# Kernel optimization log

Measured on AMD Instinct MI355X. Metric: run time of the kernel, lower is better.

Reference implementation:

```python
import jax, jax.numpy as jnp
import numpy as np

B, N, F_IN, H = 16, 2048, 6, 64
NEG_INF = -jnp.inf


def setup_inputs() -> dict:
    key = jax.random.key(0)
    ks = jax.random.split(key, 16)
    x = jax.random.normal(ks[0], (B, N, F_IN), dtype=jnp.float32)
    adj = jax.random.bernoulli(ks[1], 0.5, (B, N, N)).astype(jnp.int32)
    valid = int(N * 0.9)
    mask = jnp.broadcast_to((jnp.arange(N) < valid).astype(jnp.float32)[None, :, None], (B, N, 1))
    mask = jnp.array(mask)

    def lin(k, fi, fo):
        return jax.random.normal(k, (fi, fo), dtype=jnp.float32) / np.sqrt(fi)

    return {
        'x': x, 'adj': adj, 'mask': mask,
        'W1': lin(ks[2], F_IN, H), 'a_src1': lin(ks[3], H, 1), 'a_dst1': lin(ks[4], H, 1),
        'W2': lin(ks[5], H, H), 'a_src2': lin(ks[6], H, 1), 'a_dst2': lin(ks[7], H, 1),
        'actor_w1': lin(ks[8], H, 32), 'actor_b1': jnp.zeros((32,), jnp.float32),
        'actor_w2': lin(ks[9], 32, 1), 'actor_b2': jnp.zeros((1,), jnp.float32),
        'critic_w1': lin(ks[10], H, 32), 'critic_b1': jnp.zeros((32,), jnp.float32),
        'critic_w2': lin(ks[11], 32, 1), 'critic_b2': jnp.zeros((1,), jnp.float32),
    }


def gat_layer(x, adj, mask, W, a_src, a_dst):
    h = x @ W                                    # [B,N,H]
    s = h @ a_src                                # [B,N,1]
    d = h @ a_dst                                # [B,N,1]
    e = jax.nn.leaky_relu(s + jnp.swapaxes(d, -1, -2), 0.2)   # [B,N,N]
    e = jnp.where(adj == 0, NEG_INF, e)
    e = jnp.where(jnp.swapaxes(mask, -1, -2) == 0, NEG_INF, e)
    alpha = jnp.nan_to_num(jax.nn.softmax(e, axis=-1))
    out = alpha @ h + h
    return jax.nn.elu(out) * mask


def reference(x, adj, mask, W1, a_src1, a_dst1, W2, a_src2, a_dst2,
              actor_w1, actor_b1, actor_w2, actor_b2,
              critic_w1, critic_b1, critic_w2, critic_b2):
    h = gat_layer(x, adj, mask, W1, a_src1, a_dst1)
    h = gat_layer(h, adj, mask, W2, a_src2, a_dst2)
    logits = (jax.nn.elu(h @ actor_w1 + actor_b1) @ actor_w2 + actor_b2)[..., 0]  # [B,N]
    sum_h = h.sum(axis=1)                                   # [B,H]
    valid_counts = jnp.clip(mask.sum(axis=1), 1.0)          # [B,1]
    global_h = sum_h / valid_counts
    value = (jax.nn.elu(global_h @ critic_w1 + critic_b1) @ critic_w2 + critic_b2)[..., 0]  # [B]
    return logits, value
```

## Files before the change

kernel.cpp:

```cpp
#include <hip/hip_runtime.h>
#include <hip/hip_bf16.h>

constexpr int kB = 16;
constexpr int kN = 2048;
constexpr int kH = 64;
constexpr int kF = 6;

typedef short s16x8 __attribute__((ext_vector_type(8)));
typedef float f32x4 __attribute__((ext_vector_type(4)));

__device__ __forceinline__ unsigned short f2bf(float f) {
  __hip_bfloat16 h = __float2bfloat16(f);
  unsigned short u;
  __builtin_memcpy(&u, &h, 2);
  return u;
}

__device__ __forceinline__ float bf2f(unsigned short u) {
  unsigned int b = ((unsigned int)u) << 16;
  float f;
  __builtin_memcpy(&f, &b, 4);
  return f;
}

__device__ __forceinline__ float eluf(float x) {
  return x > 0.0f ? x : __expf(x) - 1.0f;
}

__device__ __forceinline__ unsigned int pack8(uint4 a, uint4 b) {
  unsigned int t1 = (a.y << 1) + a.x;
  unsigned int t2 = (a.w << 1) + a.z;
  unsigned int n0 = (t2 << 2) + t1;
  unsigned int u1 = (b.y << 1) + b.x;
  unsigned int u2 = (b.w << 1) + b.z;
  unsigned int n1 = (u2 << 2) + u1;
  return (n1 << 4) + n0;
}

__global__ __launch_bounds__(256) void k_embed(
    const float* __restrict__ x, const float* __restrict__ W,
    const float* __restrict__ asrc, const float* __restrict__ adst,
    const float* __restrict__ mask,
    float* __restrict__ hf, unsigned short* __restrict__ hT,
    unsigned int* __restrict__ uvpk, float* __restrict__ Rr,
    float* __restrict__ sumh,
    const float* __restrict__ W2,
    unsigned short* __restrict__ w2thi, unsigned short* __restrict__ w2tlo) {
  __shared__ float lh[64][65];
  __shared__ float psd[2][4][64];
  const int r0 = blockIdx.x * 64;
  const int b = r0 >> 11;
  const int i0 = r0 & (kN - 1);
  const int t = threadIdx.x;
  const int k = t & 63;
  const int w = t >> 6;
  if (blockIdx.x == 0) {
#pragma unroll
    for (int i = 0; i < 4; ++i) sumh[t + 256 * i] = 0.0f;
  }
  if (blockIdx.x == 1) {
#pragma unroll
    for (int i = 0; i < 16; ++i) {
      const int idx = t + 256 * i;
      const int col = idx & 63, kk = idx >> 6;
      const float wv = W2[kk * kH + col];
      const unsigned short hh = f2bf(wv);
      w2thi[col * 64 + kk] = hh;
      w2tlo[col * 64 + kk] = f2bf(wv - bf2f(hh));
    }
  }
  for (int it = 0; it < 16; ++it) {
    const int rl = w * 16 + it;
    const int row = r0 + rl;
    float h = 0.0f;
#pragma unroll
    for (int f = 0; f < kF; ++f) h = fmaf(x[(size_t)row * kF + f], W[f * kH + k], h);
    lh[rl][k] = h;
    hf[(size_t)row * kH + k] = h;
  }
  __syncthreads();
  float sp = 0.0f, dp = 0.0f;
#pragma unroll
  for (int kk = 0; kk < 16; ++kk) {
    const int k2 = w * 16 + kk;
    const float hv = lh[k][k2];
    sp = fmaf(hv, asrc[k2], sp);
    dp = fmaf(hv, adst[k2], dp);
  }
  psd[0][w][k] = sp;
  psd[1][w][k] = dp;
  __syncthreads();
  if (t < 64) {
    const float s = psd[0][0][t] + psd[0][1][t] + psd[0][2][t] + psd[0][3][t];
    const float d = psd[1][0][t] + psd[1][1][t] + psd[1][2][t] + psd[1][3][t];
    const int row = r0 + t;
    const bool mv = mask[row] != 0.0f;
    const float u = mv ? __expf(d) : 0.0f;
    const float v = mv ? __expf(0.2f * d) : 0.0f;
    uvpk[row] = ((unsigned int)f2bf(u) << 16) | f2bf(v);
    Rr[row] = __expf(-0.8f * s);
  }
  const size_t tb = (size_t)b * kN * kH + (size_t)(i0 >> 5) * 2048;
  for (int it = 0; it < 16; ++it) {
    const int kk = w * 16 + it;
    hT[tb + (size_t)(k >> 5) * 2048 + kk * 32 + (k & 31)] = f2bf(lh[k][kk]);
  }
}

template <bool PACK, bool TAIL, bool EMB>
__global__ __launch_bounds__(512) void k_attn(
    const int* __restrict__ adj, unsigned int* __restrict__ bits,
    const unsigned short* __restrict__ hT,
    const unsigned int* __restrict__ uvpk, const float* __restrict__ Rr,
    const float* __restrict__ hres, const float* __restrict__ mask,
    const float* __restrict__ aw1, const float* __restrict__ ab1,
    const float* __restrict__ aw2, const float* __restrict__ ab2,
    float* __restrict__ logits, float* __restrict__ sumh,
    const unsigned short* __restrict__ w2thi, const unsigned short* __restrict__ w2tlo,
    const float* __restrict__ asrc2, const float* __restrict__ adst2,
    float* __restrict__ h2res, unsigned short* __restrict__ hT2,
    unsigned int* __restrict__ uv2, float* __restrict__ Rr2) {
  __shared__ __align__(16) char smem[44032];
  unsigned int* uvl = (unsigned int*)smem;
  unsigned int* blw = (unsigned int*)(smem + 8192);
  unsigned short* hbase = (unsigned short*)(smem + 24832);
  char* hbc = (char*)hbase;
  int* mxp = (int*)&blw[64];
  int* rfp = (int*)&blw[129];

  const int bid0 = blockIdx.x;
  const int swz = (bid0 & 7) * 64 + (bid0 >> 3);
  const int b = swz >> 5;
  const int rb = swz & 31;
  const int row0 = rb * 64;

  const int t = threadIdx.x;
  const int wv = t >> 6;
  const int l = t & 63;
  const int r = l & 15;
  const int g = l >> 4;
  const int hf2 = wv & 1;
  const int rt = wv >> 1;
  const int rloc = rt * 16 + r;

  if (t == 0) { *mxp = -1; *rfp = 0; }

  {
    const uint4* src = (const uint4*)(uvpk + (size_t)b * kN);
    ((uint4*)uvl)[t] = src[t];
  }

  const unsigned short* hTb = hT + (size_t)b * kN * kH;
  const char* hTc = (const char*)hTb;
  *(uint4*)(hbc + t * 16) = *(const uint4*)(hTc + t * 16);
  uint4 hc0 = *(const uint4*)(hTc + 8192 + t * 16);
  uint4 hn0 = {};

  const int brow = t >> 3;
  const int bc = t & 7;
  const int bh = bc >> 2;
  const int bq4 = bc & 3;
  const int* adjLp = adj + ((size_t)b * kN + row0 + brow) * kN + bh * 32 + bq4 * 8;
  uint4 qcA = {}, qcB = {}, qnA = {}, qnB = {};
  if (PACK) {
    const uint4 a0 = *(const uint4*)(adjLp);
    const uint4 a1 = *(const uint4*)(adjLp + 4);
    ((unsigned char*)blw)[(brow * 65 + bh) * 4 + bq4] = (unsigned char)pack8(a0, a1);
    qcA = *(const uint4*)(adjLp + 64);
    qcB = *(const uint4*)(adjLp + 68);
  } else {
#pragma unroll
    for (int ii = 0; ii < 8; ++ii) {
      const int idx = ii * 512 + t;
      const int rr2 = idx >> 6, wj = idx & 63;
      blw[rr2 * 65 + wj] = bits[((size_t)b * kN + row0 + rr2) * 64 + wj];
    }
  }

  const float Ri = Rr[(size_t)b * kN + row0 + rloc];
  __syncthreads();

  {
    int lm = -1;
#pragma unroll
    for (int i = 0; i < 4; ++i)
      if (uvl[t * 4 + i] != 0u) lm = t * 4 + i;
    if (lm >= 0) atomicMax(mxp, lm);
    if (t < 64 && mask[(size_t)b * kN + row0 + t] != 0.0f) atomicOr(rfp, 1);
  }
  __syncthreads();
  const int mxv = *mxp;
  const int ntj = (mxv < 0) ? 0 : ((mxv >> 6) + 1);
  const bool ract = (*rfp != 0);

  f32x4 acc0 = {0.f, 0.f, 0.f, 0.f}, acc1 = {0.f, 0.f, 0.f, 0.f};
  f32x4 acc2 = {0.f, 0.f, 0.f, 0.f}, acc3 = {0.f, 0.f, 0.f, 0.f};
  f32x4 accz = {0.f, 0.f, 0.f, 0.f};
  s16x8 ones;
#pragma unroll
  for (int e = 0; e < 8; ++e) ones[e] = (r == 0) ? (short)0x3F80 : (short)0;

  if (ract) {
    for (int jt = 0; jt < ntj; ++jt) {
      if (jt < ntj - 2) {
        hn0 = *(const uint4*)(hTc + (size_t)(jt + 2) * 8192 + t * 16);
        if (PACK) {
          qnA = *(const uint4*)(adjLp + (size_t)(jt + 2) * 64);
          qnB = *(const uint4*)(adjLp + (size_t)(jt + 2) * 64 + 4);
        }
      }
      if (jt < ntj - 1) {
        *(uint4*)(hbc + ((jt + 1) & 1) * 8192 + t * 16) = hc0;
        if (PACK)
          ((unsigned char*)blw)[(brow * 65 + 2 * jt + 2 + bh) * 4 + bq4] =
              (unsigned char)pack8(qcA, qcB);
      }

      const unsigned int bw = blw[rloc * 65 + 2 * jt + hf2];
      const unsigned int byt = (bw >> (g * 8)) & 0xffu;
      const unsigned int* uvp = uvl + (2 * jt + hf2) * 32 + g * 8;
      const uint4 ua = *(const uint4*)uvp;
      const uint4 ub = *(const uint4*)(uvp + 4);
      union { s16x8 v; unsigned int w[4]; } afu;
      {
        const unsigned int uvw[8] = {ua.x, ua.y, ua.z, ua.w, ub.x, ub.y, ub.z, ub.w};
#pragma unroll
        for (int p = 0; p < 4; ++p) {
          unsigned int ulb = uvw[2 * p] & 0xFFFF0000u, vlb = uvw[2 * p] << 16;
          unsigned int uhb = uvw[2 * p + 1] & 0xFFFF0000u, vhb = uvw[2 * p + 1] << 16;
          float ulf, vlf, uhf, vhf;
          __builtin_memcpy(&ulf, &ulb, 4); __builtin_memcpy(&vlf, &vlb, 4);
          __builtin_memcpy(&uhf, &uhb, 4); __builtin_memcpy(&vhf, &vhb, 4);
          const float vall = fmaxf(ulf, Ri * vlf);
          const float valh = fmaxf(uhf, Ri * vhf);
          unsigned int lbits, hbits;
          __builtin_memcpy(&lbits, &vall, 4); __builtin_memcpy(&hbits, &valh, 4);
          lbits = (byt & (1u << (2 * p))) ? lbits : 0u;
          hbits = (byt & (1u << (2 * p + 1))) ? hbits : 0u;
          afu.w[p] = (hbits & 0xFFFF0000u) | (lbits >> 16);
        }
      }
      const unsigned short* cur = hbase + ((jt & 1) * 2 + hf2) * 2048 + r * 32 + g * 8;
      const s16x8 f0 = *(const s16x8*)(cur);
      const s16x8 f1 = *(const s16x8*)(cur + 512);
      const s16x8 f2 = *(const s16x8*)(cur + 1024);
      const s16x8 f3 = *(const s16x8*)(cur + 1536);

      acc0 = __builtin_amdgcn_mfma_f32_16x16x32_bf16(afu.v, f0, acc0, 0, 0, 0);
      acc1 = __builtin_amdgcn_mfma_f32_16x16x32_bf16(afu.v, f1, acc1, 0, 0, 0);
      acc2 = __builtin_amdgcn_mfma_f32_16x16x32_bf16(afu.v, f2, acc2, 0, 0, 0);
      acc3 = __builtin_amdgcn_mfma_f32_16x16x32_bf16(afu.v, f3, acc3, 0, 0, 0);
      accz = __builtin_amdgcn_mfma_f32_16x16x32_bf16(afu.v, ones, accz, 0, 0, 0);

      asm volatile("s_waitcnt lgkmcnt(0)" ::: "memory");
      __builtin_amdgcn_s_barrier();
      hc0 = hn0;
      if (PACK) { qcA = qnA; qcB = qnB; }
    }
  }

  float* psumF = (float*)(smem + 24832);
  float* zsumF = (float*)(smem + 41728);
  if (hf2 == 1) {
#pragma unroll
    for (int q = 0; q < 4; ++q) {
      const int lrow = rt * 16 + g * 4 + q;
      psumF[lrow * 66 + r + 0]  = acc0[q];
      psumF[lrow * 66 + r + 16] = acc1[q];
      psumF[lrow * 66 + r + 32] = acc2[q];
      psumF[lrow * 66 + r + 48] = acc3[q];
      if (r == 0) zsumF[lrow] = accz[q];
    }
  }
  if (PACK) {
#pragma unroll
    for (int ii = 0; ii < 8; ++ii) {
      const int idx = ii * 512 + t;
      const int rr2 = idx >> 6, wj = idx & 63;
      bits[((size_t)b * kN + row0 + rr2) * 64 + wj] = blw[rr2 * 65 + wj];
    }
  }
  __syncthreads();
  float* lhFF = (float*)smem;
  if (hf2 == 0) {
#pragma unroll
    for (int q = 0; q < 4; ++q) {
      const int lrow = rt * 16 + g * 4 + q;
      const float zq = __shfl(accz[q], (l & 48)) + zsumF[lrow];
      const float inv = (zq > 0.0f) ? 1.0f / zq : 0.0f;
      const size_t rowg = (size_t)b * kN + row0 + lrow;
      const float mk = mask[rowg];
      const float* hrp = hres + rowg * kH;
      const float o0 = eluf(fmaf(acc0[q] + psumF[lrow * 66 + r + 0],  inv, hrp[r + 0]))  * mk;
      const float o1 = eluf(fmaf(acc1[q] + psumF[lrow * 66 + r + 16], inv, hrp[r + 16])) * mk;
      const float o2 = eluf(fmaf(acc2[q] + psumF[lrow * 66 + r + 32], inv, hrp[r + 32])) * mk;
      const float o3 = eluf(fmaf(acc3[q] + psumF[lrow * 66 + r + 48], inv, hrp[r + 48])) * mk;
      lhFF[lrow * 65 + r + 0]  = o0;
      lhFF[lrow * 65 + r + 16] = o1;
      lhFF[lrow * 65 + r + 32] = o2;
      lhFF[lrow * 65 + r + 48] = o3;
    }
  }

  if (EMB) {
    __syncthreads();
    const int ntb = hf2 * 2;
    s16x8 ah[2], al[2];
    {
      const float* arow = lhFF + (rt * 16 + r) * 65;
#pragma unroll
      for (int ks = 0; ks < 2; ++ks) {
#pragma unroll
        for (int j = 0; j < 8; ++j) {
          const float v = arow[ks * 32 + g * 8 + j];
          const unsigned short hh = f2bf(v);
          ah[ks][j] = (short)hh;
          al[ks][j] = (short)f2bf(v - bf2f(hh));
        }
      }
    }
    f32x4 e0 = {0.f, 0.f, 0.f, 0.f}, e1 = {0.f, 0.f, 0.f, 0.f};
#pragma unroll
    for (int ks = 0; ks < 2; ++ks) {
      const int kof = ks * 32 + g * 8;
      {
        const s16x8 bhi = *(const s16x8*)(w2thi + (ntb * 16 + r) * 64 + kof);
        const s16x8 blo = *(const s16x8*)(w2tlo + (ntb * 16 + r) * 64 + kof);
        e0 = __builtin_amdgcn_mfma_f32_16x16x32_bf16(ah[ks], bhi, e0, 0, 0, 0);
        e0 = __builtin_amdgcn_mfma_f32_16x16x32_bf16(al[ks], bhi, e0, 0, 0, 0);
        e0 = __builtin_amdgcn_mfma_f32_16x16x32_bf16(ah[ks], blo, e0, 0, 0, 0);
      }
      {
        const s16x8 bhi = *(const s16x8*)(w2thi + ((ntb + 1) * 16 + r) * 64 + kof);
        const s16x8 blo = *(const s16x8*)(w2tlo + ((ntb + 1) * 16 + r) * 64 + kof);
        e1 = __builtin_amdgcn_mfma_f32_16x16x32_bf16(ah[ks], bhi, e1, 0, 0, 0);
        e1 = __builtin_amdgcn_mfma_f32_16x16x32_bf16(al[ks], bhi, e1, 0, 0, 0);
        e1 = __builtin_amdgcn_mfma_f32_16x16x32_bf16(ah[ks], blo, e1, 0, 0, 0);
      }
    }
    float* lh2F = (float*)(smem + 24832);
#pragma unroll
    for (int q = 0; q < 4; ++q) {
      const int lrow = rt * 16 + g * 4 + q;
      lh2F[lrow * 66 + ntb * 16 + r] = e0[q];
      lh2F[lrow * 66 + (ntb + 1) * 16 + r] = e1[q];
      const size_t rowg = (size_t)b * kN + row0 + lrow;
      h2res[rowg * kH + ntb * 16 + r] = e0[q];
      h2res[rowg * kH + (ntb + 1) * 16 + r] = e1[q];
    }
    __syncthreads();
    {
      const int ch = t >> 8;
      const int tt = t & 255;
      const int kr = tt & 31, wc = tt >> 5;
      const size_t tb2 = (size_t)b * kN * kH + (size_t)(rb * 2 + ch) * 2048;
#pragma unroll
      for (int it = 0; it < 8; ++it) {
        const int c = wc * 8 + it;
        hT2[tb2 + c * 32 + kr] = f2bf(lh2F[(ch * 32 + kr) * 66 + c]);
      }
    }
    {
      const int rw = t >> 3, c0 = (t & 7) * 8;
      float sp = 0.0f, dp = 0.0f;
#pragma unroll
      for (int j = 0; j < 8; ++j) {
        const float hv = lh2F[rw * 66 + c0 + j];
        sp = fmaf(hv, asrc2[c0 + j], sp);
        dp = fmaf(hv, adst2[c0 + j], dp);
      }
#pragma unroll
      for (int o = 4; o; o >>= 1) {
        sp += __shfl_xor(sp, o);
        dp += __shfl_xor(dp, o);
      }
      if ((t & 7) == 0) {
        const size_t rowg = (size_t)b * kN + row0 + rw;
        const bool mv = mask[rowg] != 0.0f;
        const float u = mv ? __expf(dp) : 0.0f;
        const float v = mv ? __expf(0.2f * dp) : 0.0f;
        uv2[rowg] = ((unsigned int)f2bf(u) << 16) | f2bf(v);
        Rr2[rowg] = __expf(-0.8f * sp);
      }
    }
  }

  if (TAIL) {
    __syncthreads();
    const int ln = t & 31;
    const int grp = t >> 5;
#pragma unroll
    for (int rr2 = 0; rr2 < 4; ++rr2) {
      const int lrow = grp * 4 + rr2;
      float accA = ab1[ln];
#pragma unroll 8
      for (int m = 0; m < kH; ++m) accA = fmaf(lhFF[lrow * 65 + m], aw1[m * 32 + ln], accA);
      float p = eluf(accA) * aw2[ln];
#pragma unroll
      for (int o = 16; o; o >>= 1) p += __shfl_xor(p, o, 32);
      if (ln == 0) logits[(size_t)b * kN + row0 + lrow] = p + ab2[0];
    }
    float cs = 0.0f;
    const int kcol = t & 63;
    const int seg = t >> 6;
#pragma unroll
    for (int ii = 0; ii < 8; ++ii) cs += lhFF[(seg * 8 + ii) * 65 + kcol];
    float* csF = (float*)(smem + 41984);
    csF[seg * 64 + kcol] = cs;
    __syncthreads();
    if (t < 64) {
      float s = 0.0f;
#pragma unroll
      for (int k2 = 0; k2 < 8; ++k2) s += csF[k2 * 64 + t];
      atomicAdd(&sumh[b * 64 + t], s);
    }
  }
}

__global__ __launch_bounds__(64) void k_critic2(
    const float* __restrict__ sumh, const float* __restrict__ mask,
    const float* __restrict__ cw1, const float* __restrict__ cb1,
    const float* __restrict__ cw2, const float* __restrict__ cb2,
    float* __restrict__ value) {
  __shared__ float lgh[64];
  const int b = blockIdx.x, t = threadIdx.x;
  float c = 0.0f;
#pragma unroll
  for (int ii = 0; ii < 32; ++ii) c += mask[(size_t)b * kN + t + 64 * ii];
#pragma unroll
  for (int off = 32; off; off >>= 1) c += __shfl_xor(c, off);
  lgh[t] = sumh[b * 64 + t] / fmaxf(c, 1.0f);
  __syncthreads();
  if (t < 32) {
    float acc = cb1[t];
#pragma unroll 8
    for (int m = 0; m < kH; ++m) acc = fmaf(lgh[m], cw1[m * 32 + t], acc);
    float p = eluf(acc) * cw2[t];
#pragma unroll
    for (int off = 16; off; off >>= 1) p += __shfl_xor(p, off, 32);
    if (t == 0) value[b] = p + cb2[0];
  }
}

extern "C" void kernel_launch(void* const* d_in, const int* in_sizes, int n_in,
                              void* d_out, int out_size, void* d_ws, size_t ws_size,
                              hipStream_t stream) {
  const float* x = (const float*)d_in[0];
  const int* adj = (const int*)d_in[1];
  const float* mask = (const float*)d_in[2];
  const float* W1 = (const float*)d_in[3];
  const float* asrc1 = (const float*)d_in[4];
  const float* adst1 = (const float*)d_in[5];
  const float* W2 = (const float*)d_in[6];
  const float* asrc2 = (const float*)d_in[7];
  const float* adst2 = (const float*)d_in[8];
  const float* aw1 = (const float*)d_in[9];
  const float* ab1 = (const float*)d_in[10];
  const float* aw2 = (const float*)d_in[11];
  const float* ab2 = (const float*)d_in[12];
  const float* cw1 = (const float*)d_in[13];
  const float* cb1 = (const float*)d_in[14];
  const float* cw2 = (const float*)d_in[15];
  const float* cb2 = (const float*)d_in[16];
  float* logits = (float*)d_out;
  float* value = (float*)d_out + kB * kN;

  char* ws = (char*)d_ws;
  size_t off = 0;
  auto take = [&](size_t bytes) {
    char* p = ws + off;
    off = (off + bytes + 255) & ~(size_t)255;
    return p;
  };
  unsigned int* bits = (unsigned int*)take((size_t)kB * kN * (kN / 8));
  float* hA = (float*)take((size_t)kB * kN * kH * 4);
  float* hA2 = (float*)take((size_t)kB * kN * kH * 4);
  unsigned short* hT1 = (unsigned short*)take((size_t)kB * kN * kH * 2);
  unsigned short* hT2 = (unsigned short*)take((size_t)kB * kN * kH * 2);
  unsigned int* uv1 = (unsigned int*)take((size_t)kB * kN * 4);
  unsigned int* uv2 = (unsigned int*)take((size_t)kB * kN * 4);
  float* R1 = (float*)take((size_t)kB * kN * 4);
  float* R2 = (float*)take((size_t)kB * kN * 4);
  float* sumh = (float*)take(kB * kH * 4);
  unsigned short* w2thi = (unsigned short*)take(64 * 64 * 2);
  unsigned short* w2tlo = (unsigned short*)take(64 * 64 * 2);

  k_embed<<<kB * kN / 64, 256, 0, stream>>>(x, W1, asrc1, adst1, mask, hA, hT1, uv1, R1,
                                            sumh, W2, w2thi, w2tlo);
  k_attn<true, false, true><<<kB * 32, 512, 0, stream>>>(
      adj, bits, hT1, uv1, R1, hA, mask, aw1, ab1, aw2, ab2, logits, sumh,
      w2thi, w2tlo, asrc2, adst2, hA2, hT2, uv2, R2);
  k_attn<false, true, false><<<kB * 32, 512, 0, stream>>>(
      adj, bits, hT2, uv2, R2, hA2, mask, aw1, ab1, aw2, ab2, logits, sumh,
      nullptr, nullptr, nullptr, nullptr, nullptr, nullptr, nullptr, nullptr);
  k_critic2<<<kB, 64, 0, stream>>>(sumh, mask, cw1, cb1, cw2, cb2, value);
}
```

Baseline: 110.5 us.

## Process two key tiles per barrier iteration in attention loop

After: 113.1 us. 2.4% more time.

```diff
diff --git a/kernel.cpp b/kernel.cpp
--- a/kernel.cpp
+++ b/kernel.cpp
@@ -120,11 +120,11 @@
     const float* __restrict__ asrc2, const float* __restrict__ adst2,
     float* __restrict__ h2res, unsigned short* __restrict__ hT2,
     unsigned int* __restrict__ uv2, float* __restrict__ Rr2) {
-  __shared__ __align__(16) char smem[44032];
+  __shared__ __align__(16) char smem[57600];
   unsigned int* uvl = (unsigned int*)smem;
   unsigned int* blw = (unsigned int*)(smem + 8192);
   unsigned short* hbase = (unsigned short*)(smem + 24832);
-  char* hbc = (char*)hbase;
+  const char* hbc = (const char*)hbase;
   int* mxp = (int*)&blw[64];
   int* rfp = (int*)&blw[129];
 
@@ -152,22 +152,29 @@
 
   const unsigned short* hTb = hT + (size_t)b * kN * kH;
   const char* hTc = (const char*)hTb;
-  *(uint4*)(hbc + t * 16) = *(const uint4*)(hTc + t * 16);
-  uint4 hc0 = *(const uint4*)(hTc + 8192 + t * 16);
-  uint4 hn0 = {};
+  *(uint4*)(hbase + t * 8) = *(const uint4*)(hTc + t * 16);
+  *(uint4*)(hbase + 4096 + t * 8) = *(const uint4*)(hTc + 8192 + t * 16);
+  uint4 hc0 = *(const uint4*)(hTc + 16384 + t * 16);
+  uint4 hc1 = *(const uint4*)(hTc + 16384 + 8192 + t * 16);
 
   const int brow = t >> 3;
   const int bc = t & 7;
   const int bh = bc >> 2;
   const int bq4 = bc & 3;
   const int* adjLp = adj + ((size_t)b * kN + row0 + brow) * kN + bh * 32 + bq4 * 8;
-  uint4 qcA = {}, qcB = {}, qnA = {}, qnB = {};
+  uint4 qcA0 = {}, qcA1 = {}, qcB0 = {}, qcB1 = {};
+  uint4 qnA0 = {}, qnA1 = {}, qnB0 = {}, qnB1 = {};
   if (PACK) {
     const uint4 a0 = *(const uint4*)(adjLp);
     const uint4 a1 = *(const uint4*)(adjLp + 4);
     ((unsigned char*)blw)[(brow * 65 + bh) * 4 + bq4] = (unsigned char)pack8(a0, a1);
-    qcA = *(const uint4*)(adjLp + 64);
-    qcB = *(const uint4*)(adjLp + 68);
+    const uint4 a2 = *(const uint4*)(adjLp + 64);
+    const uint4 a3 = *(const uint4*)(adjLp + 68);
+    ((unsigned char*)blw)[(brow * 65 + bh + 2) * 4 + bq4] = (unsigned char)pack8(a2, a3);
+    qcA0 = *(const uint4*)(adjLp + 128);
+    qcA1 = *(const uint4*)(adjLp + 132);
+    qcB0 = *(const uint4*)(adjLp + 192);
+    qcB1 = *(const uint4*)(adjLp + 196);
   } else {
 #pragma unroll
     for (int ii = 0; ii < 8; ++ii) {
@@ -191,6 +198,7 @@
   __syncthreads();
   const int mxv = *mxp;
   const int ntj = (mxv < 0) ? 0 : ((mxv >> 6) + 1);
+  const int nq = (ntj + 1) >> 1;
   const bool ract = (*rfp != 0);
 
   f32x4 acc0 = {0.f, 0.f, 0.f, 0.f}, acc1 = {0.f, 0.f, 0.f, 0.f};
@@ -201,61 +209,79 @@
   for (int e = 0; e < 8; ++e) ones[e] = (r == 0) ? (short)0x3F80 : (short)0;
 
   if (ract) {
-    for (int jt = 0; jt < ntj; ++jt) {
-      if (jt < ntj - 2) {
-        hn0 = *(const uint4*)(hTc + (size_t)(jt + 2) * 8192 + t * 16);
+    for (int jq = 0; jq < nq; ++jq) {
+      uint4 hn0 = {}, hn1 = {};
+      if (jq < nq - 2) {
+        const char* src = hTc + (size_t)(jq + 2) * 16384;
+        hn0 = *(const uint4*)(src + t * 16);
+        hn1 = *(const uint4*)(src + 8192 + t * 16);
         if (PACK) {
-          qnA = *(const uint4*)(adjLp + (size_t)(jt + 2) * 64);
-          qnB = *(const uint4*)(adjLp + (size_t)(jt + 2) * 64 + 4);
+          const int* ap = adjLp + (size_t)(jq + 2) * 128;
+          qnA0 = *(const uint4*)(ap);
+          qnA1 = *(const uint4*)(ap + 4);
+          qnB0 = *(const uint4*)(ap + 64);
+          qnB1 = *(const uint4*)(ap + 68);
         }
       }
-      if (jt < ntj - 1) {
-        *(uint4*)(hbc + ((jt + 1) & 1) * 8192 + t * 16) = hc0;
-        if (PACK)
-          ((unsigned char*)blw)[(brow * 65 + 2 * jt + 2 + bh) * 4 + bq4] =
-              (unsigned char)pack8(qcA, qcB);
-      }
-
-      const unsigned int bw = blw[rloc * 65 + 2 * jt + hf2];
-      const unsigned int byt = (bw >> (g * 8)) & 0xffu;
-      const unsigned int* uvp = uvl + (2 * jt + hf2) * 32 + g * 8;
-      const uint4 ua = *(const uint4*)uvp;
-      const uint4 ub = *(const uint4*)(uvp + 4);
-      union { s16x8 v; unsigned int w[4]; } afu;
-      {
-        const unsigned int uvw[8] = {ua.x, ua.y, ua.z, ua.w, ub.x, ub.y, ub.z, ub.w};
-#pragma unroll
-        for (int p = 0; p < 4; ++p) {
-          unsigned int ulb = uvw[2 * p] & 0xFFFF0000u, vlb = uvw[2 * p] << 16;
-          unsigned int uhb = uvw[2 * p + 1] & 0xFFFF0000u, vhb = uvw[2 * p + 1] << 16;
-          float ulf, vlf, uhf, vhf;
-          __builtin_memcpy(&ulf, &ulb, 4); __builtin_memcpy(&vlf, &vlb, 4);
-          __builtin_memcpy(&uhf, &uhb, 4); __builtin_memcpy(&vhf, &vhb, 4);
-          const float vall = fmaxf(ulf, Ri * vlf);
-          const float valh = fmaxf(uhf, Ri * vhf);
-          unsigned int lbits, hbits;
-          __builtin_memcpy(&lbits, &vall, 4); __builtin_memcpy(&hbits, &valh, 4);
-          lbits = (byt & (1u << (2 * p))) ? lbits : 0u;
-          hbits = (byt & (1u << (2 * p + 1))) ? hbits : 0u;
-          afu.w[p] = (hbits & 0xFFFF0000u) | (lbits >> 16);
+      if (jq < nq - 1) {
+        const int buf = (jq + 1) & 1;
+        *(uint4*)(hbase + buf * 8192 + t * 8) = hc0;
+        *(uint4*)(hbase + buf * 8192 + 4096 + t * 8) = hc1;
+        if (PACK) {
+          const int w0 = 4 * (jq + 1) + bh;
+          ((unsigned char*)blw)[(brow * 65 + w0) * 4 + bq4] =
+              (unsigned char)pack8(qcA0, qcA1);
+          ((unsigned char*)blw)[(brow * 65 + w0 + 2) * 4 + bq4] =
+              (unsigned char)pack8(qcB0, qcB1);
         }
       }
-      const unsigned short* cur = hbase + ((jt & 1) * 2 + hf2) * 2048 + r * 32 + g * 8;
-      const s16x8 f0 = *(const s16x8*)(cur);
-      const s16x8 f1 = *(const s16x8*)(cur + 512);
-      const s16x8 f2 = *(const s16x8*)(cur + 1024);
-      const s16x8 f3 = *(const s16x8*)(cur + 1536);
-
-      acc0 = __builtin_amdgcn_mfma_f32_16x16x32_bf16(afu.v, f0, acc0, 0, 0, 0);
-      acc1 = __builtin_amdgcn_mfma_f32_16x16x32_bf16(afu.v, f1, acc1, 0, 0, 0);
-      acc2 = __builtin_amdgcn_mfma_f32_16x16x32_bf16(afu.v, f2, acc2, 0, 0, 0);
-      acc3 = __builtin_amdgcn_mfma_f32_16x16x32_bf16(afu.v, f3, acc3, 0, 0, 0);
-      accz = __builtin_amdgcn_mfma_f32_16x16x32_bf16(afu.v, ones, accz, 0, 0, 0);
+
+      const int buf = jq & 1;
+#pragma unroll
+      for (int cc = 0; cc < 2; ++cc) {
+        const int ch = 4 * jq + hf2 + 2 * cc;
+        const unsigned int bw = blw[rloc * 65 + ch];
+        const unsigned int byt = (bw >> (g * 8)) & 0xffu;
+        const unsigned int* uvp = uvl + ch * 32 + g * 8;
+        const uint4 ua = *(const uint4*)uvp;
+        const uint4 ub = *(const uint4*)(uvp + 4);
+        union { s16x8 v; unsigned int w[4]; } afu;
+        {
+          const unsigned int uvw[8] = {ua.x, ua.y, ua.z, ua.w, ub.x, ub.y, ub.z, ub.w};
+#pragma unroll
+          for (int p = 0; p < 4; ++p) {
+            unsigned int ulb = uvw[2 * p] & 0xFFFF0000u, vlb = uvw[2 * p] << 16;
+            unsigned int uhb = uvw[2 * p + 1] & 0xFFFF0000u, vhb = uvw[2 * p + 1] << 16;
+            float ulf, vlf, uhf, vhf;
+            __builtin_memcpy(&ulf, &ulb, 4); __builtin_memcpy(&vlf, &vlb, 4);
+            __builtin_memcpy(&uhf, &uhb, 4); __builtin_memcpy(&vhf, &vhb, 4);
+            const float vall = fmaxf(ulf, Ri * vlf);
+            const float valh = fmaxf(uhf, Ri * vhf);
+            unsigned int lbits, hbits;
+            __builtin_memcpy(&lbits, &vall, 4); __builtin_memcpy(&hbits, &valh, 4);
+            lbits = (byt & (1u << (2 * p))) ? lbits : 0u;
+            hbits = (byt & (1u << (2 * p + 1))) ? hbits : 0u;
+            afu.w[p] = (hbits & 0xFFFF0000u) | (lbits >> 16);
+          }
+        }
+        const unsigned short* cur =
+            hbase + buf * 8192 + (hf2 + 2 * cc) * 2048 + r * 32 + g * 8;
+        const s16x8 f0 = *(const s16x8*)(cur);
+        const s16x8 f1 = *(const s16x8*)(cur + 512);
+        const s16x8 f2 = *(const s16x8*)(cur + 1024);
+        const s16x8 f3 = *(const s16x8*)(cur + 1536);
+
+        acc0 = __builtin_amdgcn_mfma_f32_16x16x32_bf16(afu.v, f0, acc0, 0, 0, 0);
+        acc1 = __builtin_amdgcn_mfma_f32_16x16x32_bf16(afu.v, f1, acc1, 0, 0, 0);
+        acc2 = __builtin_amdgcn_mfma_f32_16x16x32_bf16(afu.v, f2, acc2, 0, 0, 0);
+        acc3 = __builtin_amdgcn_mfma_f32_16x16x32_bf16(afu.v, f3, acc3, 0, 0, 0);
+        accz = __builtin_amdgcn_mfma_f32_16x16x32_bf16(afu.v, ones, accz, 0, 0, 0);
+      }
 
       asm volatile("s_waitcnt lgkmcnt(0)" ::: "memory");
       __builtin_amdgcn_s_barrier();
-      hc0 = hn0;
-      if (PACK) { qcA = qnA; qcB = qnB; }
+      hc0 = hn0; hc1 = hn1;
+      if (PACK) { qcA0 = qnA0; qcA1 = qnA1; qcB0 = qnB0; qcB1 = qnB1; }
     }
   }
 
```
